# Optimization experiments

Hardware: AMD Instinct MI355X
Metric: run time of the kernel (lower is better)

Reference implementation:

```python
import jax, jax.numpy as jnp
import numpy as np

N = 50000          # nodes
E = 800000         # edges (before self-loops)
IN_CH = 16
HID = 32
HEADS = 4
NEG_SLOPE = 0.2    # PyG GATConv default leaky_relu slope


def add_self_loops(edge_index, n):
    loops = jnp.arange(n, dtype=edge_index.dtype)
    return jnp.concatenate([edge_index, jnp.stack([loops, loops])], axis=1)


def gat_layer(x, edge_index, W, a_src, a_dst, bias, heads, out_ch, concat):
    """PyG-style GATConv: gather -> attention logits -> segment softmax over dst -> scatter."""
    n = x.shape[0]
    h = (x @ W).reshape(n, heads, out_ch)            # [N, H, C]
    src, dst = edge_index[0], edge_index[1]          # messages flow src -> dst
    alpha_src = (h * a_src).sum(-1)                  # [N, H]
    alpha_dst = (h * a_dst).sum(-1)                  # [N, H]
    e = jax.nn.leaky_relu(alpha_src[src] + alpha_dst[dst], NEG_SLOPE)  # [Etot, H]
    # numerically stable segment softmax over incoming edges of each dst node
    e_max = jax.ops.segment_max(e, dst, num_segments=n)
    e_exp = jnp.exp(e - e_max[dst])
    denom = jax.ops.segment_sum(e_exp, dst, num_segments=n)
    alpha = e_exp / (denom[dst] + 1e-16)             # [Etot, H]
    out = jax.ops.segment_sum(h[src] * alpha[..., None], dst, num_segments=n)  # [N, H, C]
    out = out.reshape(n, heads * out_ch) if concat else out.mean(axis=1)
    return out + bias


def setup_inputs() -> dict:
    key = jax.random.key(0)
    ks = jax.random.split(key, 10)
    x = jax.random.normal(ks[0], (N, IN_CH), dtype=jnp.float32)
    edge_index = jax.random.randint(ks[1], (2, E), 0, N, dtype=jnp.int64)
    s = 0.1
    W1 = jax.random.normal(ks[2], (IN_CH, HEADS * HID), dtype=jnp.float32) * s
    a_src1 = jax.random.normal(ks[3], (1, HEADS, HID), dtype=jnp.float32) * s
    a_dst1 = jax.random.normal(ks[4], (1, HEADS, HID), dtype=jnp.float32) * s
    b1 = jnp.zeros((HEADS * HID,), dtype=jnp.float32)
    W2 = jax.random.normal(ks[5], (HEADS * HID, 2), dtype=jnp.float32) * s
    a_src2 = jax.random.normal(ks[6], (1, 1, 2), dtype=jnp.float32) * s
    a_dst2 = jax.random.normal(ks[7], (1, 1, 2), dtype=jnp.float32) * s
    b2 = jnp.zeros((2,), dtype=jnp.float32)
    return {"x": x, "edge_index": edge_index,
            "W1": W1, "a_src1": a_src1, "a_dst1": a_dst1, "b1": b1,
            "W2": W2, "a_src2": a_src2, "a_dst2": a_dst2, "b2": b2}


def reference(x, edge_index, W1, a_src1, a_dst1, b1, W2, a_src2, a_dst2, b2):
    ei = add_self_loops(edge_index, x.shape[0])
    h = gat_layer(x, ei, W1, a_src1, a_dst1, b1, HEADS, HID, concat=True)
    h = jax.nn.relu(h)
    out = gat_layer(h, ei, W2, a_src2, a_dst2, b2, 1, 2, concat=False)
    return out
```

## Files before the change

### kernel.cpp

```cpp
#include <hip/hip_runtime.h>
#include <hip/hip_bf16.h>

#define N_NODES 50000
#define N_EDGES 800000
#define ETOT    (N_EDGES + N_NODES)
#define STRIDE  64
#define IN_CH   16
#define HID     32
#define HEADS   4
#define C1      (HEADS * HID)
#define NEG     0.2f
#define NSLICE  8
#define SLICE_N (N_NODES / NSLICE)
#define CAPB    112640

#define DEG_BLOCKS  ((ETOT / 4 + 255) / 256)
#define FILL2_PARTS 110
#define FILL2_BLOCKS (NSLICE * FILL2_PARTS)
#define NGROUPS     (N_NODES / 4)
#define H1_BLOCKS   2048

typedef unsigned short u16;
typedef unsigned int   u32;

__device__ __forceinline__ float bf2f(u16 b) {
    return __uint_as_float(((u32)b) << 16);
}

__device__ __forceinline__ u16 f2bf(float f) {
    __hip_bfloat16 hb = __float2bfloat16(f);
    return *(u16*)&hb;
}

__device__ __forceinline__ int clampn(int v) {
    return v < 0 ? 0 : (v >= N_NODES ? N_NODES - 1 : v);
}

__device__ __forceinline__ int eidx(const int* ei, int e, int i64, int which) {
    int v = i64 ? ei[2 * (which * N_EDGES + e)] : ei[which * N_EDGES + e];
    return clampn(v);
}

__device__ __forceinline__ float cvt(const void* src, int i, int bf) {
    return bf ? bf2f(((const u16*)src)[i]) : ((const float*)src)[i];
}

__device__ __forceinline__ int probe_bf_wave(const u16* xb) {
    int l = threadIdx.x & 63;
    int my = 0;
#pragma unroll
    for (int k = 0; k < 4; k++) {
        float f = bf2f(xb[l * 4 + k]);
        float a = fabsf(f);
        if (f == 0.0f || (a > 9.5e-7f && a < 1.05e6f)) my++;
    }
#pragma unroll
    for (int m = 32; m; m >>= 1) my += __shfl_xor(my, m);
    return __builtin_amdgcn_readfirstlane(my >= 224 ? 1 : 0);
}

__device__ __forceinline__ int probe_i64_wave(const int* ei32) {
    int l = threadIdx.x & 63;
    int nz = (l < 32 && ei32[2 * l + 1] != 0) ? 1 : 0;
#pragma unroll
    for (int m = 32; m; m >>= 1) nz += __shfl_xor(nz, m);
    return __builtin_amdgcn_readfirstlane(nz == 0 ? 1 : 0);
}

__device__ __forceinline__ void dev_bucket(const int* __restrict__ ei,
                                           u32* __restrict__ gcnt,
                                           u32* __restrict__ gbuf,
                                           u32* sbuf, u32* scnt, u32* sseg,
                                           u32* sbase, int blk) {
    int i64 = probe_i64_wave(ei);
    if (threadIdx.x < NSLICE) scnt[threadIdx.x] = 0;
    __syncthreads();
    int e0 = (blk * 256 + (int)threadIdx.x) * 4;
    int valid = (e0 < ETOT);
    int bkt[4], pos[4]; u32 pk[4];
    if (valid) {
#pragma unroll
        for (int j = 0; j < 4; j++) {
            int e = e0 + j, s, d;
            if (e < N_EDGES) { s = eidx(ei, e, i64, 0); d = eidx(ei, e, i64, 1); }
            else             { s = d = e - N_EDGES; }
            int b = d / SLICE_N;
            bkt[j] = b;
            pk[j]  = ((u32)s << 16) | (u32)(d - b * SLICE_N);
            pos[j] = (int)atomicAdd(&scnt[b], 1u);
        }
    }
    __syncthreads();
    if (threadIdx.x == 0) {
        u32 run = 0;
        for (int b = 0; b < NSLICE; b++) { sseg[b] = run; run += scnt[b]; }
    }
    __syncthreads();
    if (threadIdx.x < NSLICE)
        sbase[threadIdx.x] = atomicAdd(&gcnt[threadIdx.x * 16], scnt[threadIdx.x]);
    if (valid) {
#pragma unroll
        for (int j = 0; j < 4; j++) sbuf[sseg[bkt[j]] + pos[j]] = pk[j];
    }
    __syncthreads();
#pragma unroll
    for (int b = 0; b < NSLICE; b++) {
        u32 cb = scnt[b], sb = sseg[b], gb = sbase[b];
        for (u32 i = threadIdx.x; i < cb; i += 256) {
            u32 o = gb + i;
            if (o < CAPB) gbuf[(size_t)b * CAPB + o] = sbuf[sb + i];
        }
    }
}

__device__ __forceinline__ void dev_fill2(const u32* __restrict__ gcnt,
                                          const u32* __restrict__ gbuf,
                                          int* __restrict__ degs,
                                          u16* __restrict__ csr, int blk) {
    int s = blk & (NSLICE - 1);
    int part = blk >> 3;
    u32 cnt = gcnt[s * 16]; if (cnt > CAPB) cnt = CAPB;
    u32 i0 = ((u32)part * 256 + (u32)threadIdx.x) * 4;
    if (i0 >= cnt) return;
    const u32* buf = gbuf + (size_t)s * CAPB;
    u32 pk[4]; int nv;
    if (i0 + 4 <= cnt) {
        uint4 q = *(const uint4*)(buf + i0);
        pk[0] = q.x; pk[1] = q.y; pk[2] = q.z; pk[3] = q.w; nv = 4;
    } else {
        nv = (int)(cnt - i0);
#pragma unroll
        for (int j = 0; j < 4; j++) if (j < nv) pk[j] = buf[i0 + j];
    }
    int base = s * SLICE_N;
#pragma unroll
    for (int j = 0; j < 4; j++) {
        if (j < nv) {
            int dst = base + (int)(pk[j] & 0xFFFFu);
            u32 r = (u32)atomicAdd(&degs[dst], 1) + 1u;
            if (r < STRIDE) csr[(size_t)dst * STRIDE + r] = (u16)(pk[j] >> 16);
        }
    }
}

__launch_bounds__(256)
__global__ void k_fill2(const u32* __restrict__ gcnt, const u32* __restrict__ gbuf,
                        int* __restrict__ degs, u16* __restrict__ csr) {
    dev_fill2(gcnt, gbuf, degs, csr, blockIdx.x);
}

__device__ __forceinline__ void dev_h1(const void* __restrict__ x,
                                       const void* __restrict__ W1,
                                       const void* __restrict__ a_s,
                                       const void* __restrict__ a_d,
                                       float* __restrict__ as1,
                                       float* __restrict__ ad1, int blk) {
    int bf = probe_bf_wave((const u16*)x);
    int w = threadIdx.x >> 6, l = threadIdx.x & 63;

    float wa[IN_CH], wb[IN_CH];
    if (bf) {
        const u32* w32 = (const u32*)W1;
#pragma unroll
        for (int k = 0; k < IN_CH; k++) {
            u32 v = w32[k * 64 + l];
            wa[k] = bf2f((u16)(v & 0xFFFF));
            wb[k] = bf2f((u16)(v >> 16));
        }
    } else {
        const float2* w64 = (const float2*)W1;
#pragma unroll
        for (int k = 0; k < IN_CH; k++) {
            float2 v = w64[k * 64 + l];
            wa[k] = v.x; wb[k] = v.y;
        }
    }
    float asa, asb, ada, adb;
    if (bf) {
        u32 vs = ((const u32*)a_s)[l], vd = ((const u32*)a_d)[l];
        asa = bf2f((u16)(vs & 0xFFFF)); asb = bf2f((u16)(vs >> 16));
        ada = bf2f((u16)(vd & 0xFFFF)); adb = bf2f((u16)(vd >> 16));
    } else {
        float2 vs = ((const float2*)a_s)[l], vd = ((const float2*)a_d)[l];
        asa = vs.x; asb = vs.y; ada = vd.x; adb = vd.y;
    }

    for (int g = blk; g < NGROUPS; g += H1_BLOCKS) {
        int n = g * 4 + w;
        float xr[IN_CH];
        if (bf) {
            const uint4* xp = (const uint4*)((const u16*)x + (size_t)n * IN_CH);
            uint4 q0 = xp[0], q1 = xp[1];
            u32 qq[8] = {q0.x, q0.y, q0.z, q0.w, q1.x, q1.y, q1.z, q1.w};
#pragma unroll
            for (int k = 0; k < 8; k++) {
                xr[2 * k]     = bf2f((u16)(qq[k] & 0xFFFF));
                xr[2 * k + 1] = bf2f((u16)(qq[k] >> 16));
            }
        } else {
            const float4* xp = (const float4*)((const float*)x + (size_t)n * IN_CH);
#pragma unroll
            for (int k = 0; k < 4; k++) {
                float4 q = xp[k];
                xr[4 * k] = q.x; xr[4 * k + 1] = q.y;
                xr[4 * k + 2] = q.z; xr[4 * k + 3] = q.w;
            }
        }
        float acc0 = 0.f, acc1 = 0.f;
#pragma unroll
        for (int k = 0; k < IN_CH; k++) {
            acc0 += xr[k] * wa[k];
            acc1 += xr[k] * wb[k];
        }
        float ps = acc0 * asa + acc1 * asb;
        float pd = acc0 * ada + acc1 * adb;
#pragma unroll
        for (int m = 8; m; m >>= 1) { ps += __shfl_xor(ps, m); pd += __shfl_xor(pd, m); }
        if ((l & 15) == 0) {
            int hd = l >> 4;
            as1[n * 4 + hd] = ps;
            ad1[n * 4 + hd] = pd;
        }
    }
}

__launch_bounds__(256)
__global__ void k_bucket_h1(const void* __restrict__ x, const int* __restrict__ ei,
                            const void* __restrict__ W1, const void* __restrict__ a_s,
                            const void* __restrict__ a_d,
                            u32* __restrict__ gcnt, u32* __restrict__ gbuf,
                            float* __restrict__ as1, float* __restrict__ ad1) {
    __shared__ u32 sbuf[1024];
    __shared__ u32 scnt[NSLICE], sseg[NSLICE], sbase[NSLICE];
    if (blockIdx.x < DEG_BLOCKS) {
        dev_bucket(ei, gcnt, gbuf, sbuf, scnt, sseg, sbase, blockIdx.x);
        return;
    }
    dev_h1(x, W1, a_s, a_d, as1, ad1, blockIdx.x - DEG_BLOCKS);
}

__launch_bounds__(256)
__global__ void k_gather1(const void* __restrict__ x,
                          const int* __restrict__ degs, const u16* __restrict__ csr,
                          const float* __restrict__ as1, const float* __restrict__ ad1,
                          const void* __restrict__ W1,
                          const void* __restrict__ b1, const void* __restrict__ W2,
                          const void* __restrict__ a2s, const void* __restrict__ a2d,
                          float* __restrict__ h2, float* __restrict__ as2,
                          float* __restrict__ ad2) {
    __shared__ float xs[4][64][17];
    __shared__ float ws[4][64][4];
    int wv = threadIdx.x >> 6;
    int n  = blockIdx.x * 4 + wv;
    int l  = threadIdx.x & 63;
    int h  = l >> 4;
    int k  = l & 15;
    int g16 = l & 48;

    const u16* row = csr + (size_t)n * STRIDE;
    int se   = (int)row[l];
    int degv = degs[n];
    float4 d4 = ((const float4*)ad1)[n];

    int bf = probe_bf_wave((const u16*)x);

    int deg = degv + 1;
    deg = deg > STRIDE ? STRIDE : deg;
    int live = (l < deg);
    int sidx = (live && se < N_NODES) ? se : 0;

    if (live) {
        float4 a4 = ((const float4*)as1)[sidx];
        float xr[IN_CH];
        if (bf) {
            const uint4* xp = (const uint4*)((const u16*)x + (size_t)sidx * IN_CH);
            uint4 q0 = xp[0], q1 = xp[1];
            u32 qq[8] = {q0.x, q0.y, q0.z, q0.w, q1.x, q1.y, q1.z, q1.w};
#pragma unroll
            for (int kk = 0; kk < 8; kk++) {
                xr[2 * kk]     = bf2f((u16)(qq[kk] & 0xFFFF));
                xr[2 * kk + 1] = bf2f((u16)(qq[kk] >> 16));
            }
        } else {
            const float4* xp = (const float4*)((const float*)x + (size_t)sidx * IN_CH);
#pragma unroll
            for (int kk = 0; kk < 4; kk++) {
                float4 q = xp[kk];
                xr[4 * kk] = q.x; xr[4 * kk + 1] = q.y;
                xr[4 * kk + 2] = q.z; xr[4 * kk + 3] = q.w;
            }
        }
        float t0 = a4.x + d4.x; t0 = t0 > 0.f ? t0 : NEG * t0;
        float t1 = a4.y + d4.y; t1 = t1 > 0.f ? t1 : NEG * t1;
        float t2 = a4.z + d4.z; t2 = t2 > 0.f ? t2 : NEG * t2;
        float t3 = a4.w + d4.w; t3 = t3 > 0.f ? t3 : NEG * t3;
#pragma unroll
        for (int kk = 0; kk < IN_CH; kk++) xs[wv][l][kk] = xr[kk];
        ws[wv][l][0] = __expf(t0); ws[wv][l][1] = __expf(t1);
        ws[wv][l][2] = __expf(t2); ws[wv][l][3] = __expf(t3);
    }

    float wa[IN_CH], wb[IN_CH];
    if (bf) {
        const u32* w32 = (const u32*)W1;
#pragma unroll
        for (int kk = 0; kk < IN_CH; kk++) {
            u32 v = w32[kk * 64 + l];
            wa[kk] = bf2f((u16)(v & 0xFFFF));
            wb[kk] = bf2f((u16)(v >> 16));
        }
    } else {
        const float2* w64 = (const float2*)W1;
#pragma unroll
        for (int kk = 0; kk < IN_CH; kk++) {
            float2 v = w64[kk * 64 + l];
            wa[kk] = v.x; wb[kk] = v.y;
        }
    }
    float b1v0 = cvt(b1, 2 * l, bf),     b1v1 = cvt(b1, 2 * l + 1, bf);
    float w2a  = cvt(W2, 4 * l, bf),     w2b  = cvt(W2, 4 * l + 1, bf);
    float w2c  = cvt(W2, 4 * l + 2, bf), w2d  = cvt(W2, 4 * l + 3, bf);
    float a2s0 = cvt(a2s, 0, bf), a2s1 = cvt(a2s, 1, bf);
    float a2d0 = cvt(a2d, 0, bf), a2d1 = cvt(a2d, 1, bf);

    __syncthreads();

    float acc = 0.f, sws = 0.f;
#pragma unroll 4
    for (int j = 0; j < deg; j++) {
        float w = ws[wv][j][h];
        acc += w * xs[wv][j][k];
        sws += w;
    }
    float aggn = acc * (1.0f / sws);

    float o0 = 0.f, o1 = 0.f;
#pragma unroll
    for (int kk = 0; kk < IN_CH; kk++) {
        float a = __shfl(aggn, g16 + kk);
        o0 += a * wa[kk];
        o1 += a * wb[kk];
    }
    float v0 = o0 + b1v0;
    float v1 = o1 + b1v1;
    v0 = v0 > 0.f ? v0 : 0.f;
    v1 = v1 > 0.f ? v1 : 0.f;
    float p0 = v0 * w2a + v1 * w2c;
    float p1 = v0 * w2b + v1 * w2d;
#pragma unroll
    for (int d = 32; d; d >>= 1) { p0 += __shfl_down(p0, d); p1 += __shfl_down(p1, d); }
    if (l == 0) {
        h2[n * 2] = p0; h2[n * 2 + 1] = p1;
        as2[n] = p0 * a2s0 + p1 * a2s1;
        ad2[n] = p0 * a2d0 + p1 * a2d1;
    }
}

__launch_bounds__(256)
__global__ void k_gather2(const void* __restrict__ x,
                          const int* __restrict__ degs, const u16* __restrict__ csr,
                          const float* __restrict__ h2, const float* __restrict__ as2,
                          const float* __restrict__ ad2, const void* __restrict__ b2,
                          void* __restrict__ out) {
    int n = blockIdx.x * 16 + (threadIdx.x >> 4);
    int g = threadIdx.x & 15;
    int degv = degs[n];
    float adv = ad2[n];
    const u16* row = csr + (size_t)n * STRIDE;
    int bf = probe_bf_wave((const u16*)x);
    float a0 = 0.f, a1 = 0.f, sw = 0.f;
    int deg = degv + 1;
    deg = deg > STRIDE ? STRIDE : deg;
    for (int k = g; k < deg; k += 16) {
        int s = (int)row[k];
        float lg = as2[s] + adv;
        lg = lg > 0.f ? lg : NEG * lg;
        float w = __expf(lg);
        float2 hv = ((const float2*)h2)[s];
        a0 += w * hv.x;
        a1 += w * hv.y;
        sw += w;
    }
#pragma unroll
    for (int m = 8; m; m >>= 1) {
        a0 += __shfl_xor(a0, m); a1 += __shfl_xor(a1, m); sw += __shfl_xor(sw, m);
    }
    if (g == 0) {
        float inv = 1.0f / sw;
        float o0 = a0 * inv + cvt(b2, 0, bf);
        float o1 = a1 * inv + cvt(b2, 1, bf);
        if (bf) {
            ((u32*)out)[n] = (u32)f2bf(o0) | ((u32)f2bf(o1) << 16);
        } else {
            ((float2*)out)[n] = make_float2(o0, o1);
        }
    }
}

extern "C" void kernel_launch(void* const* d_in, const int* in_sizes, int n_in,
                              void* d_out, int out_size, void* d_ws, size_t ws_size,
                              hipStream_t stream) {
    const void* x    = d_in[0];
    const int*  ei   = (const int*)d_in[1];
    const void* W1   = d_in[2];
    const void* a_s1 = d_in[3];
    const void* a_d1 = d_in[4];
    const void* b1   = d_in[5];
    const void* W2   = d_in[6];
    const void* a_s2 = d_in[7];
    const void* a_d2 = d_in[8];
    const void* b2   = d_in[9];

    char* p = (char*)d_ws;
    int*   degs = (int*)p;     p += ((size_t)N_NODES * 4 + 255) & ~255;
    u16*   csr  = (u16*)p;     p += (size_t)N_NODES * STRIDE * 2;
    size_t init_bytes = (size_t)(p - (char*)d_ws);
    u32*   gcnt = (u32*)p;     p += 512;
    float* as1  = (float*)p;   p += (size_t)N_NODES * HEADS * 4;
    float* ad1  = (float*)p;   p += (size_t)N_NODES * HEADS * 4;
    float* h2   = (float*)p;   p += (size_t)N_NODES * 2 * 4;
    float* as2  = (float*)p;   p += (size_t)N_NODES * 4;
    float* ad2  = (float*)p;   p += (size_t)N_NODES * 4;
    u32*   gbuf = (u32*)p;     p += (size_t)NSLICE * CAPB * 4;

    hipMemsetAsync(degs, 0xFF, init_bytes, stream);
    hipMemsetAsync(gcnt, 0x00, 512, stream);

    k_bucket_h1<<<DEG_BLOCKS + H1_BLOCKS, 256, 0, stream>>>(
        x, ei, W1, a_s1, a_d1, gcnt, gbuf, as1, ad1);
    k_fill2<<<FILL2_BLOCKS, 256, 0, stream>>>(gcnt, gbuf, degs, csr);
    k_gather1<<<N_NODES / 4, 256, 0, stream>>>(
        x, degs, csr, as1, ad1, W1, b1, W2, a_s2, a_d2, h2, as2, ad2);
    k_gather2<<<N_NODES / 16, 256, 0, stream>>>(
        x, degs, csr, h2, as2, ad2, b2, d_out);
}
```

Before: 222.3 us.

## Replace two-pass bucket-then-fill CSR build with slice-filtered direct fill

The old two-phase build (bucket edges by destination slice into a global buffer, then a second kernel that fills the CSR) is replaced by a single pass. Each block re-reads one edge chunk and handles only destinations inside one of 8 slices, writing straight into degs/csr with atomics. This removes the gbuf round-trip, one kernel launch, a memset and the full CSR memset (only degs is reset now). In exchange every edge is read 8 times, and atomics are spread across all destinations rather than being slice-local in time.

```diff
diff --git a/kernel.cpp b/kernel.cpp
--- a/kernel.cpp
+++ b/kernel.cpp
@@ -12,11 +12,9 @@
 #define NEG     0.2f
 #define NSLICE  8
 #define SLICE_N (N_NODES / NSLICE)
-#define CAPB    112640
 
 #define DEG_BLOCKS  ((ETOT / 4 + 255) / 256)
-#define FILL2_PARTS 110
-#define FILL2_BLOCKS (NSLICE * FILL2_PARTS)
+#define FILL_BLOCKS (NSLICE * DEG_BLOCKS)
 #define NGROUPS     (N_NODES / 4)
 #define H1_BLOCKS   2048
 
@@ -67,86 +65,29 @@
     return __builtin_amdgcn_readfirstlane(nz == 0 ? 1 : 0);
 }
 
-__device__ __forceinline__ void dev_bucket(const int* __restrict__ ei,
-                                           u32* __restrict__ gcnt,
-                                           u32* __restrict__ gbuf,
-                                           u32* sbuf, u32* scnt, u32* sseg,
-                                           u32* sbase, int blk) {
+__device__ __forceinline__ void dev_degfill(const int* __restrict__ ei,
+                                            int* __restrict__ degs,
+                                            u16* __restrict__ csr, int blk) {
+    int slice = blk & (NSLICE - 1);
+    int chunk = blk >> 3;
     int i64 = probe_i64_wave(ei);
-    if (threadIdx.x < NSLICE) scnt[threadIdx.x] = 0;
-    __syncthreads();
-    int e0 = (blk * 256 + (int)threadIdx.x) * 4;
-    int valid = (e0 < ETOT);
-    int bkt[4], pos[4]; u32 pk[4];
-    if (valid) {
-#pragma unroll
-        for (int j = 0; j < 4; j++) {
-            int e = e0 + j, s, d;
-            if (e < N_EDGES) { s = eidx(ei, e, i64, 0); d = eidx(ei, e, i64, 1); }
-            else             { s = d = e - N_EDGES; }
-            int b = d / SLICE_N;
-            bkt[j] = b;
-            pk[j]  = ((u32)s << 16) | (u32)(d - b * SLICE_N);
-            pos[j] = (int)atomicAdd(&scnt[b], 1u);
-        }
-    }
-    __syncthreads();
-    if (threadIdx.x == 0) {
-        u32 run = 0;
-        for (int b = 0; b < NSLICE; b++) { sseg[b] = run; run += scnt[b]; }
-    }
-    __syncthreads();
-    if (threadIdx.x < NSLICE)
-        sbase[threadIdx.x] = atomicAdd(&gcnt[threadIdx.x * 16], scnt[threadIdx.x]);
-    if (valid) {
-#pragma unroll
-        for (int j = 0; j < 4; j++) sbuf[sseg[bkt[j]] + pos[j]] = pk[j];
-    }
-    __syncthreads();
-#pragma unroll
-    for (int b = 0; b < NSLICE; b++) {
-        u32 cb = scnt[b], sb = sseg[b], gb = sbase[b];
-        for (u32 i = threadIdx.x; i < cb; i += 256) {
-            u32 o = gb + i;
-            if (o < CAPB) gbuf[(size_t)b * CAPB + o] = sbuf[sb + i];
-        }
-    }
-}
-
-__device__ __forceinline__ void dev_fill2(const u32* __restrict__ gcnt,
-                                          const u32* __restrict__ gbuf,
-                                          int* __restrict__ degs,
-                                          u16* __restrict__ csr, int blk) {
-    int s = blk & (NSLICE - 1);
-    int part = blk >> 3;
-    u32 cnt = gcnt[s * 16]; if (cnt > CAPB) cnt = CAPB;
-    u32 i0 = ((u32)part * 256 + (u32)threadIdx.x) * 4;
-    if (i0 >= cnt) return;
-    const u32* buf = gbuf + (size_t)s * CAPB;
-    u32 pk[4]; int nv;
-    if (i0 + 4 <= cnt) {
-        uint4 q = *(const uint4*)(buf + i0);
-        pk[0] = q.x; pk[1] = q.y; pk[2] = q.z; pk[3] = q.w; nv = 4;
-    } else {
-        nv = (int)(cnt - i0);
-#pragma unroll
-        for (int j = 0; j < 4; j++) if (j < nv) pk[j] = buf[i0 + j];
-    }
-    int base = s * SLICE_N;
+    int e0 = (chunk * 256 + (int)threadIdx.x) * 4;
+    if (e0 >= ETOT) return;
+    int lo = slice * SLICE_N, hi = lo + SLICE_N;
+    int s[4], d[4];
 #pragma unroll
     for (int j = 0; j < 4; j++) {
-        if (j < nv) {
-            int dst = base + (int)(pk[j] & 0xFFFFu);
-            u32 r = (u32)atomicAdd(&degs[dst], 1) + 1u;
-            if (r < STRIDE) csr[(size_t)dst * STRIDE + r] = (u16)(pk[j] >> 16);
-        }
-    }
-}
-
-__launch_bounds__(256)
-__global__ void k_fill2(const u32* __restrict__ gcnt, const u32* __restrict__ gbuf,
-                        int* __restrict__ degs, u16* __restrict__ csr) {
-    dev_fill2(gcnt, gbuf, degs, csr, blockIdx.x);
+        int e = e0 + j;
+        if (e < N_EDGES) { s[j] = eidx(ei, e, i64, 0); d[j] = eidx(ei, e, i64, 1); }
+        else             { s[j] = d[j] = e - N_EDGES; }
+    }
+#pragma unroll
+    for (int j = 0; j < 4; j++) {
+        if (d[j] >= lo && d[j] < hi) {
+            u32 r = (u32)atomicAdd(&degs[d[j]], 1) + 1u;
+            if (r < STRIDE) csr[(size_t)d[j] * STRIDE + r] = (u16)s[j];
+        }
+    }
 }
 
 __device__ __forceinline__ void dev_h1(const void* __restrict__ x,
@@ -225,18 +166,13 @@
 }
 
 __launch_bounds__(256)
-__global__ void k_bucket_h1(const void* __restrict__ x, const int* __restrict__ ei,
-                            const void* __restrict__ W1, const void* __restrict__ a_s,
-                            const void* __restrict__ a_d,
-                            u32* __restrict__ gcnt, u32* __restrict__ gbuf,
-                            float* __restrict__ as1, float* __restrict__ ad1) {
-    __shared__ u32 sbuf[1024];
-    __shared__ u32 scnt[NSLICE], sseg[NSLICE], sbase[NSLICE];
-    if (blockIdx.x < DEG_BLOCKS) {
-        dev_bucket(ei, gcnt, gbuf, sbuf, scnt, sseg, sbase, blockIdx.x);
-        return;
-    }
-    dev_h1(x, W1, a_s, a_d, as1, ad1, blockIdx.x - DEG_BLOCKS);
+__global__ void k_fill_h1(const void* __restrict__ x, const int* __restrict__ ei,
+                          const void* __restrict__ W1, const void* __restrict__ a_s,
+                          const void* __restrict__ a_d,
+                          int* __restrict__ degs, u16* __restrict__ csr,
+                          float* __restrict__ as1, float* __restrict__ ad1) {
+    if (blockIdx.x < FILL_BLOCKS) { dev_degfill(ei, degs, csr, blockIdx.x); return; }
+    dev_h1(x, W1, a_s, a_d, as1, ad1, blockIdx.x - FILL_BLOCKS);
 }
 
 __launch_bounds__(256)
@@ -414,21 +350,16 @@
     char* p = (char*)d_ws;
     int*   degs = (int*)p;     p += ((size_t)N_NODES * 4 + 255) & ~255;
     u16*   csr  = (u16*)p;     p += (size_t)N_NODES * STRIDE * 2;
-    size_t init_bytes = (size_t)(p - (char*)d_ws);
-    u32*   gcnt = (u32*)p;     p += 512;
     float* as1  = (float*)p;   p += (size_t)N_NODES * HEADS * 4;
     float* ad1  = (float*)p;   p += (size_t)N_NODES * HEADS * 4;
     float* h2   = (float*)p;   p += (size_t)N_NODES * 2 * 4;
     float* as2  = (float*)p;   p += (size_t)N_NODES * 4;
     float* ad2  = (float*)p;   p += (size_t)N_NODES * 4;
-    u32*   gbuf = (u32*)p;     p += (size_t)NSLICE * CAPB * 4;
-
-    hipMemsetAsync(degs, 0xFF, init_bytes, stream);
-    hipMemsetAsync(gcnt, 0x00, 512, stream);
-
-    k_bucket_h1<<<DEG_BLOCKS + H1_BLOCKS, 256, 0, stream>>>(
-        x, ei, W1, a_s1, a_d1, gcnt, gbuf, as1, ad1);
-    k_fill2<<<FILL2_BLOCKS, 256, 0, stream>>>(gcnt, gbuf, degs, csr);
+
+    hipMemsetAsync(degs, 0xFF, (size_t)N_NODES * 4, stream);
+
+    k_fill_h1<<<FILL_BLOCKS + H1_BLOCKS, 256, 0, stream>>>(
+        x, ei, W1, a_s1, a_d1, degs, csr, as1, ad1);
     k_gather1<<<N_NODES / 4, 256, 0, stream>>>(
         x, degs, csr, as1, ad1, W1, b1, W2, a_s2, a_d2, h2, as2, ad2);
     k_gather2<<<N_NODES / 16, 256, 0, stream>>>(
```

Result: faster. 206.7 us (-7.0%).
